# Kernel optimization log

Measured on AMD Instinct MI355X. Metric: run time of the kernel, lower is better.

Reference implementation:

```python
import jax, jax.numpy as jnp
import numpy as np

B, F = 64, 2048

def setup_inputs() -> dict:
    key = jax.random.key(0)
    k1, k2, k3, k4, k5 = jax.random.split(key, 5)
    scale = 1.0 / np.sqrt(F)
    return {
        "x": jax.random.normal(k1, (B, F), dtype=jnp.float32),
        "feature_mask": jax.random.randint(k2, (B, F), 0, 2, dtype=jnp.int32),
        "Wq": jax.random.normal(k3, (F, F), dtype=jnp.float32) * scale,
        "Wk": jax.random.normal(k4, (F, F), dtype=jnp.float32) * scale,
        "Wv": jax.random.normal(k5, (F, F), dtype=jnp.float32) * scale,
    }

def reference(x, feature_mask, Wq, Wk, Wv):
    # nn.Linear(bias=False): y = x @ W.T
    q = x @ Wq.T  # (B, F)
    k = x @ Wk.T
    v = x @ Wv.T
    # outer-product scores: (B, F, F) = q[:, :, None] * k[:, None, :]
    scores = q[:, :, None] * k[:, None, :]
    # mask broadcast over query dim (unsqueeze(1) in torch)
    scores = jnp.where(feature_mask[:, None, :] == 0, -1e9, scores)
    attn = jax.nn.softmax(scores, axis=-1)  # (B, F, F)
    attended = jnp.einsum("bfg,bg->bf", attn, v)  # (B, F)
    return attended
```

## Files before the change

kernel.cpp:

```cpp
#include <hip/hip_runtime.h>
#include <hip/hip_bf16.h>

#define B 64
#define F 2048
#define BN 64
#define BK 32
#define KSPLIT 8
#define KCHUNK (F / KSPLIT)
#define NITER (KCHUNK / BK)
#define LDSW 40
#define GS 4
#define NSEG 2
#define SEGG 1024

typedef __attribute__((ext_vector_type(8))) short bf16x8;
typedef __attribute__((ext_vector_type(4))) float f32x4;

#define PART_FLOATS (KSPLIT * 3 * B * F)
#define KVC_FLOATS (B * 2 * F)

#if __has_builtin(__builtin_amdgcn_exp2f)
#define EXP2(x) __builtin_amdgcn_exp2f(x)
#else
#define EXP2(x) exp2f(x)
#endif

__device__ __forceinline__ void split2(float f0, float f1, int& hi, int& lo) {
  union { float f; unsigned u; } a, b;
  a.f = f0; b.f = f1;
  union { unsigned u; float f; } ha, hb;
  ha.u = a.u & 0xFFFF0000u;
  hb.u = b.u & 0xFFFF0000u;
  union { float f; unsigned u; } la, lb;
  la.f = f0 - ha.f;
  lb.f = f1 - hb.f;
  hi = (int)__builtin_amdgcn_perm(b.u, a.u, 0x07060302u);
  lo = (int)__builtin_amdgcn_perm(lb.u, la.u, 0x07060302u);
}

__global__ __launch_bounds__(256) void qkv_gemm_kernel(
    const float* __restrict__ x, const float* __restrict__ Wq,
    const float* __restrict__ Wk, const float* __restrict__ Wv,
    float* __restrict__ part) {
  __shared__ __align__(16) short xs_hi[2][B][LDSW];
  __shared__ __align__(16) short xs_lo[2][B][LDSW];
  __shared__ __align__(16) short ws_hi[2][BN][LDSW];
  __shared__ __align__(16) short ws_lo[2][BN][LDSW];

  const int tid  = threadIdx.x;
  const int f0   = blockIdx.x * BN;
  const int kb   = blockIdx.y;
  const int mat  = blockIdx.z;
  const float* W = (mat == 0) ? Wq : (mat == 1) ? Wk : Wv;

  const int lrow = tid >> 2;
  const int lc0  = (tid & 3) << 3;

  const int wave = tid >> 6;
  const int lane = tid & 63;
  const int l15  = lane & 15;
  const int quad = lane >> 4;

  const float* xg = x + lrow * F + kb * KCHUNK + lc0;
  const float* wg = W + (f0 + lrow) * F + kb * KCHUNK + lc0;

  f32x4 acc[4];
#pragma unroll
  for (int i = 0; i < 4; ++i) acc[i] = (f32x4){0.f, 0.f, 0.f, 0.f};

  float4 px[2][2], pw[2][2];
  px[0][0] = *(const float4*)(xg);
  px[0][1] = *(const float4*)(xg + 4);
  pw[0][0] = *(const float4*)(wg);
  pw[0][1] = *(const float4*)(wg + 4);

#pragma unroll
  for (int it = 0; it < NITER; ++it) {
    const int cur = it & 1, nxt = cur ^ 1;
    if (it + 1 < NITER) {
      const float* xp = xg + (it + 1) * BK;
      const float* wp = wg + (it + 1) * BK;
      px[nxt][0] = *(const float4*)(xp);
      px[nxt][1] = *(const float4*)(xp + 4);
      pw[nxt][0] = *(const float4*)(wp);
      pw[nxt][1] = *(const float4*)(wp + 4);
    }
    int4 xh, xl, wh, wl;
    split2(px[cur][0].x, px[cur][0].y, xh.x, xl.x);
    split2(px[cur][0].z, px[cur][0].w, xh.y, xl.y);
    split2(px[cur][1].x, px[cur][1].y, xh.z, xl.z);
    split2(px[cur][1].z, px[cur][1].w, xh.w, xl.w);
    split2(pw[cur][0].x, pw[cur][0].y, wh.x, wl.x);
    split2(pw[cur][0].z, pw[cur][0].w, wh.y, wl.y);
    split2(pw[cur][1].x, pw[cur][1].y, wh.z, wl.z);
    split2(pw[cur][1].z, pw[cur][1].w, wh.w, wl.w);
    *(int4*)&xs_hi[cur][lrow][lc0] = xh;
    *(int4*)&xs_lo[cur][lrow][lc0] = xl;
    *(int4*)&ws_hi[cur][lrow][lc0] = wh;
    *(int4*)&ws_lo[cur][lrow][lc0] = wl;
    __syncthreads();

    bf16x8 a_hi = *(const bf16x8*)&xs_hi[cur][(wave << 4) + l15][quad << 3];
    bf16x8 a_lo = *(const bf16x8*)&xs_lo[cur][(wave << 4) + l15][quad << 3];
#pragma unroll
    for (int nt = 0; nt < 4; ++nt) {
      bf16x8 b_hi = *(const bf16x8*)&ws_hi[cur][(nt << 4) + l15][quad << 3];
      bf16x8 b_lo = *(const bf16x8*)&ws_lo[cur][(nt << 4) + l15][quad << 3];
      acc[nt] = __builtin_amdgcn_mfma_f32_16x16x32_bf16(a_hi, b_hi, acc[nt], 0, 0, 0);
      acc[nt] = __builtin_amdgcn_mfma_f32_16x16x32_bf16(a_hi, b_lo, acc[nt], 0, 0, 0);
      acc[nt] = __builtin_amdgcn_mfma_f32_16x16x32_bf16(a_lo, b_hi, acc[nt], 0, 0, 0);
    }
  }

  float* outp = part + (size_t)(kb * 3 + mat) * B * F;
#pragma unroll
  for (int nt = 0; nt < 4; ++nt) {
    int f = f0 + (nt << 4) + l15;
#pragma unroll
    for (int r = 0; r < 4; ++r) {
      int brow = (wave << 4) + (quad << 2) + r;
      outp[brow * F + f] = acc[nt][r];
    }
  }
}

__global__ __launch_bounds__(256) void prep_kernel(
    const float* __restrict__ part, const int* __restrict__ mask,
    float* __restrict__ kvc, float* __restrict__ vsum2,
    float* __restrict__ kmax2, float* __restrict__ kmin2,
    int* __restrict__ cnt2) {
  __shared__ int cnt;
  __shared__ float svs[4], smx[4], smn[4];

  const int b    = blockIdx.x;
  const int seg  = blockIdx.y;
  const int tid  = threadIdx.x;
  const int wave = tid >> 6;
  const int lane = tid & 63;

  if (tid == 0) cnt = 0;
  __syncthreads();

  const int g0 = seg * SEGG + (tid << 2);
  float4 kq = {0.f, 0.f, 0.f, 0.f}, vq = {0.f, 0.f, 0.f, 0.f};
#pragma unroll
  for (int p = 0; p < KSPLIT; ++p) {
    const float4 kp = *(const float4*)&part[((p * 3 + 1) * B + b) * F + g0];
    const float4 vp = *(const float4*)&part[((p * 3 + 2) * B + b) * F + g0];
    kq.x += kp.x; kq.y += kp.y; kq.z += kp.z; kq.w += kp.w;
    vq.x += vp.x; vq.y += vp.y; vq.z += vp.z; vq.w += vp.w;
  }
  float vs = (vq.x + vq.y) + (vq.z + vq.w);

  const int4 m4 = *(const int4*)&mask[b * F + g0];
  const float kk[4] = {kq.x, kq.y, kq.z, kq.w};
  const float vv[4] = {vq.x, vq.y, vq.z, vq.w};
  const bool  act[4] = {m4.x != 0, m4.y != 0, m4.z != 0, m4.w != 0};

  unsigned long long bal[4];
  int tot = 0;
#pragma unroll
  for (int j = 0; j < 4; ++j) {
    bal[j] = __ballot(act[j]);
    tot += __popcll(bal[j]);
  }
  int base = 0;
  if (lane == 0) base = atomicAdd(&cnt, tot);
  base = __shfl(base, 0);

  float* kvb = kvc + (size_t)b * 2 * F + seg * 2 * SEGG;
  const unsigned long long ltm = (1ull << lane) - 1ull;
  float kmx = -3.4e38f, kmn = 3.4e38f;
  int off = base;
#pragma unroll
  for (int j = 0; j < 4; ++j) {
    if (act[j]) {
      int pos = off + __popcll(bal[j] & ltm);
      *(float2*)&kvb[2 * pos] = (float2){kk[j], vv[j]};
      kmx = fmaxf(kmx, kk[j]);
      kmn = fminf(kmn, kk[j]);
    }
    off += __popcll(bal[j]);
  }

#pragma unroll
  for (int o = 32; o > 0; o >>= 1) {
    vs += __shfl_xor(vs, o);
    kmx = fmaxf(kmx, __shfl_xor(kmx, o));
    kmn = fminf(kmn, __shfl_xor(kmn, o));
  }
  if (lane == 0) { svs[wave] = vs; smx[wave] = kmx; smn[wave] = kmn; }
  __syncthreads();
  if (tid == 0) {
    vsum2[b * NSEG + seg] = svs[0] + svs[1] + svs[2] + svs[3];
    kmax2[b * NSEG + seg] = fmaxf(fmaxf(smx[0], smx[1]), fmaxf(smx[2], smx[3]));
    kmin2[b * NSEG + seg] = fminf(fminf(smn[0], smn[1]), fminf(smn[2], smn[3]));
    cnt2[b * NSEG + seg]  = cnt;
  }
}

__global__ __launch_bounds__(1024, 8) void attn_kernel(
    const float* __restrict__ part, const float* __restrict__ kvc,
    const float* __restrict__ vsum2, const float* __restrict__ kmax2,
    const float* __restrict__ kmin2, const int* __restrict__ cnt2,
    float* __restrict__ out) {
  __shared__ float rn[GS][256];
  __shared__ float rd[GS][256];

  const int b     = blockIdx.x;
  const int tid   = threadIdx.x;
  const int fl    = tid & 255;
  const int slice = __builtin_amdgcn_readfirstlane(tid >> 8);
  const int fi    = blockIdx.y * 256 + fl;

  float s = 0.f;
#pragma unroll
  for (int p = 0; p < KSPLIT; ++p) s += part[((p * 3 + 0) * B + b) * F + fi];

  int cnts[NSEG];
  float km = -3.4e38f, kn = 3.4e38f;
  int ntot = 0;
  float vstot = 0.f;
#pragma unroll
  for (int g2 = 0; g2 < NSEG; ++g2) {
    cnts[g2] = cnt2[b * NSEG + g2];
    ntot += cnts[g2];
    km = fmaxf(km, kmax2[b * NSEG + g2]);
    kn = fminf(kn, kmin2[b * NSEG + g2]);
    vstot += vsum2[b * NSEG + g2];
  }

  const float L2E = 1.44269504088896f;
  const float se  = s * L2E;
  const float nm2 = -se * ((s >= 0.f) ? km : kn);

  float n0 = 0.f, n1 = 0.f, n2 = 0.f, n3 = 0.f;
  float d0 = 0.f, d1 = 0.f, d2 = 0.f, d3 = 0.f;
  const float* kvbase = kvc + (size_t)b * 2 * F;
#pragma unroll
  for (int seg = 0; seg < NSEG; ++seg) {
    const int cnt   = cnts[seg];
    const int quads = cnt >> 1;
    const int q0 = (slice * quads) / GS;
    const int q1 = ((slice + 1) * quads) / GS;
    const float4* bp = (const float4*)(kvbase + seg * 2 * SEGG);
    int q = q0;
    for (; q + 4 <= q1; q += 4) {
      float4 p0 = bp[q];
      float4 p1 = bp[q + 1];
      float4 p2 = bp[q + 2];
      float4 p3 = bp[q + 3];
      float e0 = EXP2(fmaf(se, p0.x, nm2));
      float e1 = EXP2(fmaf(se, p0.z, nm2));
      float e2 = EXP2(fmaf(se, p1.x, nm2));
      float e3 = EXP2(fmaf(se, p1.z, nm2));
      float e4 = EXP2(fmaf(se, p2.x, nm2));
      float e5 = EXP2(fmaf(se, p2.z, nm2));
      float e6 = EXP2(fmaf(se, p3.x, nm2));
      float e7 = EXP2(fmaf(se, p3.z, nm2));
      n0 = fmaf(e0, p0.y, n0); d0 += e0;
      n1 = fmaf(e1, p0.w, n1); d1 += e1;
      n2 = fmaf(e2, p1.y, n2); d2 += e2;
      n3 = fmaf(e3, p1.w, n3); d3 += e3;
      n0 = fmaf(e4, p2.y, n0); d0 += e4;
      n1 = fmaf(e5, p2.w, n1); d1 += e5;
      n2 = fmaf(e6, p3.y, n2); d2 += e6;
      n3 = fmaf(e7, p3.w, n3); d3 += e7;
    }
    for (; q < q1; ++q) {
      float4 p0 = bp[q];
      float e0 = EXP2(fmaf(se, p0.x, nm2));
      float e1 = EXP2(fmaf(se, p0.z, nm2));
      n0 = fmaf(e0, p0.y, n0); d0 += e0;
      n1 = fmaf(e1, p0.w, n1); d1 += e1;
    }
    if ((slice == GS - 1) && (cnt & 1)) {
      float2 p = *(const float2*)(kvbase + seg * 2 * SEGG + 2 * (cnt - 1));
      float e = EXP2(fmaf(se, p.x, nm2));
      n2 = fmaf(e, p.y, n2); d2 += e;
    }
  }
  rn[slice][fl] = (n0 + n1) + (n2 + n3);
  rd[slice][fl] = (d0 + d1) + (d2 + d3);
  __syncthreads();
  if (slice == 0) {
    float N = (rn[0][fl] + rn[1][fl]) + (rn[2][fl] + rn[3][fl]);
    float D = (rd[0][fl] + rd[1][fl]) + (rd[2][fl] + rd[3][fl]);
    out[b * F + fi] = (ntot > 0) ? (N / D) : (vstot * (1.0f / (float)F));
  }
}

extern "C" void kernel_launch(void* const* d_in, const int* in_sizes, int n_in,
                              void* d_out, int out_size, void* d_ws, size_t ws_size,
                              hipStream_t stream) {
  const float* x  = (const float*)d_in[0];
  const int* mask = (const int*)d_in[1];
  const float* Wq = (const float*)d_in[2];
  const float* Wk = (const float*)d_in[3];
  const float* Wv = (const float*)d_in[4];
  float* out = (float*)d_out;

  float* part  = (float*)d_ws;
  float* kvc   = part + PART_FLOATS;
  float* vsum2 = kvc + KVC_FLOATS;
  float* kmx2  = vsum2 + B * NSEG;
  float* kmn2  = kmx2 + B * NSEG;
  int*   cnt2  = (int*)(kmn2 + B * NSEG);

  dim3 gg(F / BN, KSPLIT, 3);
  qkv_gemm_kernel<<<gg, 256, 0, stream>>>(x, Wq, Wk, Wv, part);
  dim3 gp(B, NSEG);
  prep_kernel<<<gp, 256, 0, stream>>>(part, mask, kvc, vsum2, kmx2, kmn2, cnt2);
  dim3 ga(B, F / 256);
  attn_kernel<<<ga, 1024, 0, stream>>>(part, kvc, vsum2, kmx2, kmn2, cnt2, out);
}
```

Measured before the change: 122.0 us.

## Halve GEMM N-tile and K-split, reduce Q partials in prep kernel

The QKV GEMM tile width drops from 64 to 32 columns and the K-split from 8 to 4. The grid size stays the same, but each block runs longer K loops, and the partial-sum buffer traffic written and re-read by later kernels is halved. The Q partial-sum reduction moves from the attention kernel into the prep kernel, which writes a reduced q buffer. That buffer is read once per element instead of the attention kernel summing the partials across all its slice threads. The cost is lower MFMA reuse per loaded x tile and an extra B×F write.

```diff
diff --git a/kernel.cpp b/kernel.cpp
--- a/kernel.cpp
+++ b/kernel.cpp
@@ -3,9 +3,9 @@
 
 #define B 64
 #define F 2048
-#define BN 64
+#define BN 32
 #define BK 32
-#define KSPLIT 8
+#define KSPLIT 4
 #define KCHUNK (F / KSPLIT)
 #define NITER (KCHUNK / BK)
 #define LDSW 40
@@ -18,6 +18,7 @@
 
 #define PART_FLOATS (KSPLIT * 3 * B * F)
 #define KVC_FLOATS (B * 2 * F)
+#define QS_FLOATS (B * F)
 
 #if __has_builtin(__builtin_amdgcn_exp2f)
 #define EXP2(x) __builtin_amdgcn_exp2f(x)
@@ -55,6 +56,8 @@
 
   const int lrow = tid >> 2;
   const int lc0  = (tid & 3) << 3;
+  const int wrow = tid >> 3;
+  const int wc0  = (tid & 7) << 2;
 
   const int wave = tid >> 6;
   const int lane = tid & 63;
@@ -62,48 +65,44 @@
   const int quad = lane >> 4;
 
   const float* xg = x + lrow * F + kb * KCHUNK + lc0;
-  const float* wg = W + (f0 + lrow) * F + kb * KCHUNK + lc0;
-
-  f32x4 acc[4];
-#pragma unroll
-  for (int i = 0; i < 4; ++i) acc[i] = (f32x4){0.f, 0.f, 0.f, 0.f};
-
-  float4 px[2][2], pw[2][2];
+  const float* wg = W + (f0 + wrow) * F + kb * KCHUNK + wc0;
+
+  f32x4 acc[2];
+#pragma unroll
+  for (int i = 0; i < 2; ++i) acc[i] = (f32x4){0.f, 0.f, 0.f, 0.f};
+
+  float4 px[2][2], pw[2];
   px[0][0] = *(const float4*)(xg);
   px[0][1] = *(const float4*)(xg + 4);
-  pw[0][0] = *(const float4*)(wg);
-  pw[0][1] = *(const float4*)(wg + 4);
+  pw[0]    = *(const float4*)(wg);
 
 #pragma unroll
   for (int it = 0; it < NITER; ++it) {
     const int cur = it & 1, nxt = cur ^ 1;
     if (it + 1 < NITER) {
       const float* xp = xg + (it + 1) * BK;
-      const float* wp = wg + (it + 1) * BK;
       px[nxt][0] = *(const float4*)(xp);
       px[nxt][1] = *(const float4*)(xp + 4);
-      pw[nxt][0] = *(const float4*)(wp);
-      pw[nxt][1] = *(const float4*)(wp + 4);
-    }
-    int4 xh, xl, wh, wl;
+      pw[nxt]    = *(const float4*)(wg + (it + 1) * BK);
+    }
+    int4 xh, xl;
+    int2 wh, wl;
     split2(px[cur][0].x, px[cur][0].y, xh.x, xl.x);
     split2(px[cur][0].z, px[cur][0].w, xh.y, xl.y);
     split2(px[cur][1].x, px[cur][1].y, xh.z, xl.z);
     split2(px[cur][1].z, px[cur][1].w, xh.w, xl.w);
-    split2(pw[cur][0].x, pw[cur][0].y, wh.x, wl.x);
-    split2(pw[cur][0].z, pw[cur][0].w, wh.y, wl.y);
-    split2(pw[cur][1].x, pw[cur][1].y, wh.z, wl.z);
-    split2(pw[cur][1].z, pw[cur][1].w, wh.w, wl.w);
+    split2(pw[cur].x, pw[cur].y, wh.x, wl.x);
+    split2(pw[cur].z, pw[cur].w, wh.y, wl.y);
     *(int4*)&xs_hi[cur][lrow][lc0] = xh;
     *(int4*)&xs_lo[cur][lrow][lc0] = xl;
-    *(int4*)&ws_hi[cur][lrow][lc0] = wh;
-    *(int4*)&ws_lo[cur][lrow][lc0] = wl;
+    *(int2*)&ws_hi[cur][wrow][wc0] = wh;
+    *(int2*)&ws_lo[cur][wrow][wc0] = wl;
     __syncthreads();
 
     bf16x8 a_hi = *(const bf16x8*)&xs_hi[cur][(wave << 4) + l15][quad << 3];
     bf16x8 a_lo = *(const bf16x8*)&xs_lo[cur][(wave << 4) + l15][quad << 3];
 #pragma unroll
-    for (int nt = 0; nt < 4; ++nt) {
+    for (int nt = 0; nt < 2; ++nt) {
       bf16x8 b_hi = *(const bf16x8*)&ws_hi[cur][(nt << 4) + l15][quad << 3];
       bf16x8 b_lo = *(const bf16x8*)&ws_lo[cur][(nt << 4) + l15][quad << 3];
       acc[nt] = __builtin_amdgcn_mfma_f32_16x16x32_bf16(a_hi, b_hi, acc[nt], 0, 0, 0);
@@ -114,7 +113,7 @@
 
   float* outp = part + (size_t)(kb * 3 + mat) * B * F;
 #pragma unroll
-  for (int nt = 0; nt < 4; ++nt) {
+  for (int nt = 0; nt < 2; ++nt) {
     int f = f0 + (nt << 4) + l15;
 #pragma unroll
     for (int r = 0; r < 4; ++r) {
@@ -126,9 +125,9 @@
 
 __global__ __launch_bounds__(256) void prep_kernel(
     const float* __restrict__ part, const int* __restrict__ mask,
-    float* __restrict__ kvc, float* __restrict__ vsum2,
-    float* __restrict__ kmax2, float* __restrict__ kmin2,
-    int* __restrict__ cnt2) {
+    float* __restrict__ kvc, float* __restrict__ qs,
+    float* __restrict__ vsum2, float* __restrict__ kmax2,
+    float* __restrict__ kmin2, int* __restrict__ cnt2) {
   __shared__ int cnt;
   __shared__ float svs[4], smx[4], smn[4];
 
@@ -142,14 +141,18 @@
   __syncthreads();
 
   const int g0 = seg * SEGG + (tid << 2);
+  float4 qq = {0.f, 0.f, 0.f, 0.f};
   float4 kq = {0.f, 0.f, 0.f, 0.f}, vq = {0.f, 0.f, 0.f, 0.f};
 #pragma unroll
   for (int p = 0; p < KSPLIT; ++p) {
+    const float4 qp = *(const float4*)&part[((p * 3 + 0) * B + b) * F + g0];
     const float4 kp = *(const float4*)&part[((p * 3 + 1) * B + b) * F + g0];
     const float4 vp = *(const float4*)&part[((p * 3 + 2) * B + b) * F + g0];
+    qq.x += qp.x; qq.y += qp.y; qq.z += qp.z; qq.w += qp.w;
     kq.x += kp.x; kq.y += kp.y; kq.z += kp.z; kq.w += kp.w;
     vq.x += vp.x; vq.y += vp.y; vq.z += vp.z; vq.w += vp.w;
   }
+  *(float4*)&qs[b * F + g0] = qq;
   float vs = (vq.x + vq.y) + (vq.z + vq.w);
 
   const int4 m4 = *(const int4*)&mask[b * F + g0];
@@ -200,7 +203,7 @@
 }
 
 __global__ __launch_bounds__(1024, 8) void attn_kernel(
-    const float* __restrict__ part, const float* __restrict__ kvc,
+    const float* __restrict__ qs, const float* __restrict__ kvc,
     const float* __restrict__ vsum2, const float* __restrict__ kmax2,
     const float* __restrict__ kmin2, const int* __restrict__ cnt2,
     float* __restrict__ out) {
@@ -213,9 +216,7 @@
   const int slice = __builtin_amdgcn_readfirstlane(tid >> 8);
   const int fi    = blockIdx.y * 256 + fl;
 
-  float s = 0.f;
-#pragma unroll
-  for (int p = 0; p < KSPLIT; ++p) s += part[((p * 3 + 0) * B + b) * F + fi];
+  const float s = qs[b * F + fi];
 
   int cnts[NSEG];
   float km = -3.4e38f, kn = 3.4e38f;
@@ -302,7 +303,8 @@
 
   float* part  = (float*)d_ws;
   float* kvc   = part + PART_FLOATS;
-  float* vsum2 = kvc + KVC_FLOATS;
+  float* qs    = kvc + KVC_FLOATS;
+  float* vsum2 = qs + QS_FLOATS;
   float* kmx2  = vsum2 + B * NSEG;
   float* kmn2  = kmx2 + B * NSEG;
   int*   cnt2  = (int*)(kmn2 + B * NSEG);
@@ -310,7 +312,7 @@
   dim3 gg(F / BN, KSPLIT, 3);
   qkv_gemm_kernel<<<gg, 256, 0, stream>>>(x, Wq, Wk, Wv, part);
   dim3 gp(B, NSEG);
-  prep_kernel<<<gp, 256, 0, stream>>>(part, mask, kvc, vsum2, kmx2, kmn2, cnt2);
+  prep_kernel<<<gp, 256, 0, stream>>>(part, mask, kvc, qs, vsum2, kmx2, kmn2, cnt2);
   dim3 ga(B, F / 256);
-  attn_kernel<<<ga, 1024, 0, stream>>>(part, kvc, vsum2, kmx2, kmn2, cnt2, out);
-}
+  attn_kernel<<<ga, 1024, 0, stream>>>(qs, kvc, vsum2, kmx2, kmn2, cnt2, out);
+}
```

After: 122.6 us. Within noise of the previous version (+0.5%).
